# Kernel optimization log

Hardware: AMD Instinct MI355X
Metric: run time of the kernel (lower is better)

Reference implementation:

```python
import jax, jax.numpy as jnp
import numpy as np
import math

B, N, DIM = 16, 1024, 384
DEPTH, HEADS, DH = 6, 6, 64
INNER = HEADS * DH          # 384
MLP = 1536
LN_EPS = 1e-5


def setup_inputs() -> dict:
    key = jax.random.key(0)
    ks = jax.random.split(key, 7)
    s = 0.02
    x = jax.random.normal(ks[0], (B, N, DIM), dtype=jnp.float32)
    ln1_g = jnp.ones((DEPTH, DIM), jnp.float32)
    ln1_b = jnp.zeros((DEPTH, DIM), jnp.float32)
    qkv_w = jax.random.normal(ks[1], (DEPTH, DIM, 3 * INNER), jnp.float32) * s
    temp = jnp.full((DEPTH,), math.log(DH ** -0.5), jnp.float32)
    out_w = jax.random.normal(ks[2], (DEPTH, INNER, DIM), jnp.float32) * s
    out_b = jnp.zeros((DEPTH, DIM), jnp.float32)
    ln2_g = jnp.ones((DEPTH, DIM), jnp.float32)
    ln2_b = jnp.zeros((DEPTH, DIM), jnp.float32)
    ff_w1 = jax.random.normal(ks[3], (DEPTH, DIM, MLP), jnp.float32) * s
    ff_b1 = jnp.zeros((DEPTH, MLP), jnp.float32)
    ff_w2 = jax.random.normal(ks[4], (DEPTH, MLP, DIM), jnp.float32) * s
    ff_b2 = jnp.zeros((DEPTH, DIM), jnp.float32)
    return dict(x=x, ln1_g=ln1_g, ln1_b=ln1_b, qkv_w=qkv_w, temp=temp,
                out_w=out_w, out_b=out_b, ln2_g=ln2_g, ln2_b=ln2_b,
                ff_w1=ff_w1, ff_b1=ff_b1, ff_w2=ff_w2, ff_b2=ff_b2)


def _ln(x, g, b):
    m = jnp.mean(x, axis=-1, keepdims=True)
    v = jnp.var(x, axis=-1, keepdims=True)
    return (x - m) * jax.lax.rsqrt(v + LN_EPS) * g + b


def reference(x, ln1_g, ln1_b, qkv_w, temp, out_w, out_b,
              ln2_g, ln2_b, ff_w1, ff_b1, ff_w2, ff_b2):
    neg = -jnp.finfo(x.dtype).max
    eye = jnp.eye(N, dtype=bool)

    def step(x, p):
        g1, b1, wqkv, t, wo, bo, g2, b2, w1, bb1, w2, bb2 = p
        # --- PreNorm + LSA attention ---
        h = _ln(x, g1, b1)
        qkv = h @ wqkv                              # [B, N, 3*INNER]
        q, k, v = jnp.split(qkv, 3, axis=-1)
        split_heads = lambda a: a.reshape(B, N, HEADS, DH).transpose(0, 2, 1, 3)
        q, k, v = split_heads(q), split_heads(k), split_heads(v)
        dots = jnp.einsum('bhnd,bhmd->bhnm', q, k) * jnp.exp(t)
        dots = jnp.where(eye, neg, dots)            # mask diagonal (LSA)
        attn = jax.nn.softmax(dots, axis=-1)
        o = jnp.einsum('bhnm,bhmd->bhnd', attn, v)
        o = o.transpose(0, 2, 1, 3).reshape(B, N, INNER)
        x = x + o @ wo + bo
        # --- PreNorm + FeedForward (exact GELU) ---
        h2 = _ln(x, g2, b2)
        ff = jax.nn.gelu(h2 @ w1 + bb1, approximate=False) @ w2 + bb2
        x = x + ff
        return x, None

    params = (ln1_g, ln1_b, qkv_w, temp, out_w, out_b,
              ln2_g, ln2_b, ff_w1, ff_b1, ff_w2, ff_b2)
    x, _ = jax.lax.scan(step, x, params)
    return x
```

## Files before the change

### kernel.cpp

```cpp
#include <hip/hip_runtime.h>
#include <hip/hip_bf16.h>
#include <math.h>

#define B_     16
#define NTOK   1024
#define DIM_   384
#define DEPTH_ 6
#define HEADS_ 6
#define DH_    64
#define MLP_   1536
#define MTOT   (B_ * NTOK)
#define NBH    (B_ * HEADS_)
#define QKV_PLANE ((size_t)NBH * NTOK * DH_)

typedef unsigned short u16;
typedef unsigned int u32;
typedef short short8 __attribute__((ext_vector_type(8)));
typedef float f32x4 __attribute__((ext_vector_type(4)));

static __device__ __forceinline__ u16 f2b(float f) {
    __hip_bfloat16 h = __float2bfloat16(f);
    return *reinterpret_cast<u16*>(&h);
}

#define GLOAD_LDS16(gp, lp)                                                     \
    __builtin_amdgcn_global_load_lds(                                           \
        (const __attribute__((address_space(1))) void*)(gp),                    \
        (__attribute__((address_space(3))) void*)(lp), 16, 0, 0)

__launch_bounds__(256)
__global__ void transpose_w_kernel(const float* __restrict__ W, u16* __restrict__ WT,
                                   int K, int N) {
    const int layer = blockIdx.z;
    W  += (size_t)layer * K * N;
    WT += (size_t)layer * K * N;
    __shared__ u16 tile[64 * 72];
    const int t = threadIdx.x;
    const int k0 = blockIdx.x * 64, n0 = blockIdx.y * 64;
    const int row = t >> 2, cs = (t & 3) * 16;
    const float4* src = reinterpret_cast<const float4*>(W + (size_t)(k0 + row) * N + n0 + cs);
#pragma unroll
    for (int i = 0; i < 4; i++) {
        float4 f = src[i];
        tile[row * 72 + cs + i * 4 + 0] = f2b(f.x);
        tile[row * 72 + cs + i * 4 + 1] = f2b(f.y);
        tile[row * 72 + cs + i * 4 + 2] = f2b(f.z);
        tile[row * 72 + cs + i * 4 + 3] = f2b(f.w);
    }
    __syncthreads();
    const int nrow = row, ks = cs;
    u16 vals[16] __attribute__((aligned(16)));
#pragma unroll
    for (int e = 0; e < 16; e++) vals[e] = tile[(ks + e) * 72 + nrow];
    u16* dst = WT + (size_t)(n0 + nrow) * K + k0 + ks;
    *reinterpret_cast<short8*>(dst)     = *reinterpret_cast<short8*>(&vals[0]);
    *reinterpret_cast<short8*>(dst + 8) = *reinterpret_cast<short8*>(&vals[8]);
}

__launch_bounds__(256)
__global__ void ln_kernel(const float* __restrict__ x, const float* __restrict__ g,
                          const float* __restrict__ b, u16* __restrict__ h) {
    const int tok  = blockIdx.x * 4 + (threadIdx.x >> 6);
    const int lane = threadIdx.x & 63;
    const float* xr = x + (size_t)tok * DIM_;
    float v[6];
    float s = 0.f;
#pragma unroll
    for (int i = 0; i < 6; i++) { v[i] = xr[lane + i * 64]; s += v[i]; }
#pragma unroll
    for (int m = 1; m < 64; m <<= 1) s += __shfl_xor(s, m);
    const float mean = s * (1.f / 384.f);
    float qs = 0.f;
#pragma unroll
    for (int i = 0; i < 6; i++) { float d = v[i] - mean; qs += d * d; }
#pragma unroll
    for (int m = 1; m < 64; m <<= 1) qs += __shfl_xor(qs, m);
    const float inv = rsqrtf(qs * (1.f / 384.f) + 1e-5f);
    u16* hr = h + (size_t)tok * DIM_;
#pragma unroll
    for (int i = 0; i < 6; i++) {
        const int c = lane + i * 64;
        hr[c] = f2b((v[i] - mean) * inv * g[c] + b[c]);
    }
}

enum { EPI_QKV = 0, EPI_RES = 1, EPI_GELU = 2 };

template <int EPI>
__launch_bounds__(256)
__global__ void gemm_kernel(const u16* __restrict__ A, const u16* __restrict__ BT, int K,
                            const float* __restrict__ bias, const float* __restrict__ resid,
                            float* __restrict__ outf, u16* __restrict__ outb, int ldc,
                            u16* __restrict__ qkv_base) {
    __shared__ u16 As[128 * 32];
    __shared__ u16 Bs[128 * 32];
    const int t = threadIdx.x;
    const int lane = t & 63, w = t >> 6;
    const int wm = w >> 1, wn = w & 1;
    const int m0 = blockIdx.x * 128, n0 = blockIdx.y * 128;

    f32x4 acc[4][4] = {};

    const int c0 = w * 2, c1 = w * 2 + 1;
    const int seg = (lane & 3) * 8;
    const u16* agp0 = A  + (size_t)(m0 + c0 * 16 + (lane >> 2)) * K + seg;
    const u16* agp1 = A  + (size_t)(m0 + c1 * 16 + (lane >> 2)) * K + seg;
    const u16* bgp0 = BT + (size_t)(n0 + c0 * 16 + (lane >> 2)) * K + seg;
    const u16* bgp1 = BT + (size_t)(n0 + c1 * 16 + (lane >> 2)) * K + seg;
    u16* asl0 = &As[c0 * 512];
    u16* asl1 = &As[c1 * 512];
    u16* bsl0 = &Bs[c0 * 512];
    u16* bsl1 = &Bs[c1 * 512];

    for (int kk = 0; kk < K; kk += 32) {
        __syncthreads();
        GLOAD_LDS16(agp0 + kk, asl0);
        GLOAD_LDS16(agp1 + kk, asl1);
        GLOAD_LDS16(bgp0 + kk, bsl0);
        GLOAD_LDS16(bgp1 + kk, bsl1);
        __syncthreads();
        short8 af[4], bf[4];
#pragma unroll
        for (int i = 0; i < 4; i++)
            af[i] = *reinterpret_cast<const short8*>(
                &As[(wm * 64 + i * 16 + (lane & 15)) * 32 + (lane >> 4) * 8]);
#pragma unroll
        for (int j = 0; j < 4; j++)
            bf[j] = *reinterpret_cast<const short8*>(
                &Bs[(wn * 64 + j * 16 + (lane & 15)) * 32 + (lane >> 4) * 8]);
#pragma unroll
        for (int i = 0; i < 4; i++)
#pragma unroll
            for (int j = 0; j < 4; j++)
                acc[i][j] = __builtin_amdgcn_mfma_f32_16x16x32_bf16(af[i], bf[j], acc[i][j], 0, 0, 0);
    }

    const int rbase = (lane >> 4) * 4;
    const int cb = lane & 15;
#pragma unroll
    for (int i = 0; i < 4; i++) {
#pragma unroll
        for (int j = 0; j < 4; j++) {
            if constexpr (EPI == EPI_QKV) {
                const int c = n0 + wn * 64 + j * 16 + cb;
                const int which = c / 384;
                const int cc = c - which * 384;
                const int head = cc >> 6, dh = cc & 63;
                const int nb = m0 + wm * 64 + i * 16 + rbase;
                const int b = nb >> 10, nt = nb & 1023;
                const size_t bh = (size_t)(b * HEADS_ + head);
                if (which == 2) {
                    u16 pk[4] __attribute__((aligned(8)));
#pragma unroll
                    for (int r = 0; r < 4; r++) pk[r] = f2b(acc[i][j][r]);
                    const int nsw = (nt & ~63) | ((((nt >> 3) & 7) ^ (dh & 7)) << 3) | (nt & 7);
                    *reinterpret_cast<uint2*>(
                        &qkv_base[2 * QKV_PLANE + bh * 65536 + (size_t)dh * 1024 + nsw]) =
                        *reinterpret_cast<uint2*>(pk);
                } else if (which == 1) {
#pragma unroll
                    for (int r = 0; r < 4; r++) {
                        const int n = nt + r;
                        const int dsw = (((dh >> 3) ^ (n & 7)) << 3) | (dh & 7);
                        qkv_base[QKV_PLANE + bh * 65536 + (size_t)n * 64 + dsw] =
                            f2b(acc[i][j][r]);
                    }
                } else {
#pragma unroll
                    for (int r = 0; r < 4; r++)
                        qkv_base[bh * 65536 + (size_t)(nt + r) * 64 + dh] = f2b(acc[i][j][r]);
                }
            } else {
#pragma unroll
                for (int r = 0; r < 4; r++) {
                    const int m = m0 + wm * 64 + i * 16 + rbase + r;
                    const int c = n0 + wn * 64 + j * 16 + cb;
                    const float val = acc[i][j][r];
                    if constexpr (EPI == EPI_RES) {
                        outf[(size_t)m * ldc + c] = resid[(size_t)m * ldc + c] + bias[c] + val;
                    } else {
                        const float xg = val + bias[c];
                        const float ge = 0.5f * xg * (1.0f + erff(xg * 0.70710678118f));
                        outb[(size_t)m * ldc + c] = f2b(ge);
                    }
                }
            }
        }
    }
}

__launch_bounds__(256)
__global__ void attn_kernel(const u16* __restrict__ q, const u16* __restrict__ k,
                            const u16* __restrict__ v, const float* __restrict__ temp,
                            u16* __restrict__ o) {
    __shared__ u16 Kt[64 * 64];
    __shared__ u16 Vt[64 * 64];
    __shared__ u16 Ps[4][16 * 80];
    const int t = threadIdx.x, lane = t & 63, w = t >> 6;
    const int g8 = lane >> 4, qi = lane & 15;
    const int bh = blockIdx.x, q0 = blockIdx.y * 64;
    const float scale2 = __expf(temp[0]) * 1.4426950408889634f;
    const size_t base = (size_t)bh * (NTOK * DH_);

    short8 bq[2];
#pragma unroll
    for (int s = 0; s < 2; s++)
        bq[s] = *reinterpret_cast<const short8*>(
            &q[base + (size_t)(q0 + w * 16 + qi) * 64 + s * 32 + g8 * 8]);

    float m_s = -3.0e38f, l_s = 0.f;
    f32x4 accO[4] = {};
    const int qglob = q0 + w * 16 + qi;

    const int srow = w * 8 + (lane >> 3);
    const int schunk = (lane & 7) * 8;
    const u16* kg0 = k + base + (size_t)srow * 64 + schunk;
    const u16* vg0 = v + base + (size_t)srow * 1024 + schunk;
    u16* klds = &Kt[w * 512];
    u16* vlds = &Vt[w * 512];

    for (int j0 = 0; j0 < NTOK; j0 += 64) {
        __syncthreads();
        GLOAD_LDS16(kg0 + (size_t)j0 * 64,            klds);
        GLOAD_LDS16(kg0 + (size_t)j0 * 64 + 32 * 64,  klds + 2048);
        GLOAD_LDS16(vg0 + j0,                         vlds);
        GLOAD_LDS16(vg0 + j0 + 32 * 1024,             vlds + 2048);
        __syncthreads();

        f32x4 sf[4] = {};
#pragma unroll
        for (int c = 0; c < 4; c++) {
            const int krow = c * 16 + qi;
#pragma unroll
            for (int s = 0; s < 2; s++) {
                short8 af = *reinterpret_cast<const short8*>(
                    &Kt[krow * 64 + (((s * 4 + g8) ^ (krow & 7)) << 3)]);
                sf[c] = __builtin_amdgcn_mfma_f32_16x16x32_bf16(af, bq[s], sf[c], 0, 0, 0);
            }
        }

        float p[4][4];
        float vmax = -3.0e38f;
        if (j0 == q0) {
#pragma unroll
            for (int c = 0; c < 4; c++)
#pragma unroll
                for (int r = 0; r < 4; r++) {
                    float sv = sf[c][r] * scale2;
                    if (j0 + c * 16 + g8 * 4 + r == qglob) sv = -3.0e37f;
                    p[c][r] = sv;
                    vmax = fmaxf(vmax, sv);
                }
        } else {
#pragma unroll
            for (int c = 0; c < 4; c++)
#pragma unroll
                for (int r = 0; r < 4; r++) {
                    const float sv = sf[c][r] * scale2;
                    p[c][r] = sv;
                    vmax = fmaxf(vmax, sv);
                }
        }
        vmax = fmaxf(vmax, __shfl_xor(vmax, 16));
        vmax = fmaxf(vmax, __shfl_xor(vmax, 32));

        if (!__all(vmax - m_s <= 11.0f)) {
            const float mnew = fmaxf(m_s, vmax);
            const float alpha = exp2f(m_s - mnew);
            m_s = mnew;
            l_s *= alpha;
#pragma unroll
            for (int r = 0; r < 4; r++) {
                const float a_r = __shfl(alpha, g8 * 4 + r, 64);
#pragma unroll
                for (int g = 0; g < 4; g++) accO[g][r] *= a_r;
            }
        }

        float tsum = 0.f;
#pragma unroll
        for (int c = 0; c < 4; c++)
#pragma unroll
            for (int r = 0; r < 4; r++) {
                const float pe = exp2f(p[c][r] - m_s);
                p[c][r] = pe;
                tsum += pe;
            }
        tsum += __shfl_xor(tsum, 16);
        tsum += __shfl_xor(tsum, 32);
        l_s += tsum;

#pragma unroll
        for (int c = 0; c < 4; c++) {
            u32 lo = (u32)f2b(p[c][0]) | ((u32)f2b(p[c][1]) << 16);
            u32 hi = (u32)f2b(p[c][2]) | ((u32)f2b(p[c][3]) << 16);
            uint2 pr; pr.x = lo; pr.y = hi;
            *reinterpret_cast<uint2*>(&Ps[w][qi * 80 + c * 16 + g8 * 4]) = pr;
        }

#pragma unroll
        for (int s = 0; s < 2; s++) {
            short8 ap = *reinterpret_cast<const short8*>(&Ps[w][qi * 80 + s * 32 + g8 * 8]);
#pragma unroll
            for (int g = 0; g < 4; g++) {
                const int vrow = g * 16 + qi;
                short8 bv = *reinterpret_cast<const short8*>(
                    &Vt[vrow * 64 + (((s * 4 + g8) ^ (vrow & 7)) << 3)]);
                accO[g] = __builtin_amdgcn_mfma_f32_16x16x32_bf16(ap, bv, accO[g], 0, 0, 0);
            }
        }
    }

    const int bidx = bh / HEADS_, head = bh % HEADS_;
#pragma unroll
    for (int r = 0; r < 4; r++) {
        const float li = __shfl(l_s, g8 * 4 + r, 64);
        const float linv = 1.f / li;
        const int n = q0 + w * 16 + g8 * 4 + r;
#pragma unroll
        for (int g = 0; g < 4; g++) {
            const int dh = g * 16 + qi;
            o[((size_t)(bidx * NTOK + n)) * DIM_ + head * DH_ + dh] = f2b(accO[g][r] * linv);
        }
    }
}

extern "C" void kernel_launch(void* const* d_in, const int* in_sizes, int n_in,
                              void* d_out, int out_size, void* d_ws, size_t ws_size,
                              hipStream_t stream) {
    const float* x_in  = (const float*)d_in[0];
    const float* ln1_g = (const float*)d_in[1];
    const float* ln1_b = (const float*)d_in[2];
    const float* qkv_w = (const float*)d_in[3];
    const float* temp  = (const float*)d_in[4];
    const float* out_w = (const float*)d_in[5];
    const float* out_b = (const float*)d_in[6];
    const float* ln2_g = (const float*)d_in[7];
    const float* ln2_b = (const float*)d_in[8];
    const float* ff_w1 = (const float*)d_in[9];
    const float* ff_b1 = (const float*)d_in[10];
    const float* ff_w2 = (const float*)d_in[11];
    const float* ff_b2 = (const float*)d_in[12];

    char* ws = (char*)d_ws;
    size_t off = 0;
    auto alloc = [&](size_t bytes) -> void* {
        void* p = ws + off;
        off += (bytes + 255) & ~(size_t)255;
        return p;
    };
    u16* wt_qkv = (u16*)alloc((size_t)DEPTH_ * 1152 * 384 * 2);
    u16* wt_out = (u16*)alloc((size_t)DEPTH_ * 384 * 384 * 2);
    u16* wt_ff1 = (u16*)alloc((size_t)DEPTH_ * 1536 * 384 * 2);
    u16* wt_ff2 = (u16*)alloc((size_t)DEPTH_ * 384 * 1536 * 2);
    u16* H      = (u16*)alloc((size_t)MTOT * DIM_ * 2);
    u16* QKV    = (u16*)alloc((size_t)MTOT * MLP_ * 2);
    u16* MID    = QKV;

    float* X = (float*)d_out;

    hipMemcpyAsync(X, x_in, (size_t)MTOT * DIM_ * sizeof(float),
                   hipMemcpyDeviceToDevice, stream);

    transpose_w_kernel<<<dim3(6, 18, DEPTH_), 256, 0, stream>>>(qkv_w, wt_qkv, 384, 1152);
    transpose_w_kernel<<<dim3(6, 6, DEPTH_), 256, 0, stream>>>(out_w, wt_out, 384, 384);
    transpose_w_kernel<<<dim3(6, 24, DEPTH_), 256, 0, stream>>>(ff_w1, wt_ff1, 384, 1536);
    transpose_w_kernel<<<dim3(24, 6, DEPTH_), 256, 0, stream>>>(ff_w2, wt_ff2, 1536, 384);

    for (int layer = 0; layer < DEPTH_; layer++) {
        ln_kernel<<<4096, 256, 0, stream>>>(X, ln1_g + layer * DIM_, ln1_b + layer * DIM_, H);
        gemm_kernel<EPI_QKV><<<dim3(128, 9), 256, 0, stream>>>(
            H, wt_qkv + (size_t)layer * 1152 * 384, 384,
            nullptr, nullptr, nullptr, nullptr, 0, QKV);
        attn_kernel<<<dim3(96, 16), 256, 0, stream>>>(
            QKV, QKV + QKV_PLANE, QKV + 2 * QKV_PLANE, temp + layer, H);
        gemm_kernel<EPI_RES><<<dim3(128, 3), 256, 0, stream>>>(
            H, wt_out + (size_t)layer * 384 * 384, 384,
            out_b + layer * DIM_, X, X, nullptr, DIM_, nullptr);
        ln_kernel<<<4096, 256, 0, stream>>>(X, ln2_g + layer * DIM_, ln2_b + layer * DIM_, H);
        gemm_kernel<EPI_GELU><<<dim3(128, 12), 256, 0, stream>>>(
            H, wt_ff1 + (size_t)layer * 1536 * 384, 384,
            ff_b1 + layer * MLP_, nullptr, nullptr, MID, MLP_, nullptr);
        gemm_kernel<EPI_RES><<<dim3(128, 3), 256, 0, stream>>>(
            MID, wt_ff2 + (size_t)layer * 384 * 1536, 1536,
            ff_b2 + layer * DIM_, X, X, nullptr, DIM_, nullptr);
    }
}
```

Baseline: 1.388 ms.

## Multi-buffer LDS loads in GEMM and attention to overlap global loads with MFMA

After: 1.371 ms. Within noise of the previous version (-1.2%).

```diff
diff --git a/kernel.cpp b/kernel.cpp
--- a/kernel.cpp
+++ b/kernel.cpp
@@ -27,6 +27,13 @@
     __builtin_amdgcn_global_load_lds(                                           \
         (const __attribute__((address_space(1))) void*)(gp),                    \
         (__attribute__((address_space(3))) void*)(lp), 16, 0, 0)
+
+#define WAIT_VM(N)                                                              \
+    do { asm volatile("s_waitcnt vmcnt(" #N ")" ::: "memory");                  \
+         __builtin_amdgcn_sched_barrier(0); } while (0)
+#define WAIT_LGKM0()                                                            \
+    do { asm volatile("s_waitcnt lgkmcnt(0)" ::: "memory");                     \
+         __builtin_amdgcn_sched_barrier(0); } while (0)
 
 __launch_bounds__(256)
 __global__ void transpose_w_kernel(const float* __restrict__ W, u16* __restrict__ WT,
@@ -92,8 +99,8 @@
                             const float* __restrict__ bias, const float* __restrict__ resid,
                             float* __restrict__ outf, u16* __restrict__ outb, int ldc,
                             u16* __restrict__ qkv_base) {
-    __shared__ u16 As[128 * 32];
-    __shared__ u16 Bs[128 * 32];
+    __shared__ u16 As[3][4096];
+    __shared__ u16 Bs[3][4096];
     const int t = threadIdx.x;
     const int lane = t & 63, w = t >> 6;
     const int wm = w >> 1, wn = w & 1;
@@ -101,38 +108,55 @@
 
     f32x4 acc[4][4] = {};
 
-    const int c0 = w * 2, c1 = w * 2 + 1;
+    const int c0p = w * 1024, c1p = w * 1024 + 512;
     const int seg = (lane & 3) * 8;
-    const u16* agp0 = A  + (size_t)(m0 + c0 * 16 + (lane >> 2)) * K + seg;
-    const u16* agp1 = A  + (size_t)(m0 + c1 * 16 + (lane >> 2)) * K + seg;
-    const u16* bgp0 = BT + (size_t)(n0 + c0 * 16 + (lane >> 2)) * K + seg;
-    const u16* bgp1 = BT + (size_t)(n0 + c1 * 16 + (lane >> 2)) * K + seg;
-    u16* asl0 = &As[c0 * 512];
-    u16* asl1 = &As[c1 * 512];
-    u16* bsl0 = &Bs[c0 * 512];
-    u16* bsl1 = &Bs[c1 * 512];
-
-    for (int kk = 0; kk < K; kk += 32) {
-        __syncthreads();
-        GLOAD_LDS16(agp0 + kk, asl0);
-        GLOAD_LDS16(agp1 + kk, asl1);
-        GLOAD_LDS16(bgp0 + kk, bsl0);
-        GLOAD_LDS16(bgp1 + kk, bsl1);
-        __syncthreads();
+    const u16* agp0 = A  + (size_t)(m0 + (w * 2 + 0) * 16 + (lane >> 2)) * K + seg;
+    const u16* agp1 = A  + (size_t)(m0 + (w * 2 + 1) * 16 + (lane >> 2)) * K + seg;
+    const u16* bgp0 = BT + (size_t)(n0 + (w * 2 + 0) * 16 + (lane >> 2)) * K + seg;
+    const u16* bgp1 = BT + (size_t)(n0 + (w * 2 + 1) * 16 + (lane >> 2)) * K + seg;
+
+    const int T = K >> 5;
+    GLOAD_LDS16(agp0,      &As[0][c0p]);
+    GLOAD_LDS16(agp1,      &As[0][c1p]);
+    GLOAD_LDS16(bgp0,      &Bs[0][c0p]);
+    GLOAD_LDS16(bgp1,      &Bs[0][c1p]);
+    GLOAD_LDS16(agp0 + 32, &As[1][c0p]);
+    GLOAD_LDS16(agp1 + 32, &As[1][c1p]);
+    GLOAD_LDS16(bgp0 + 32, &Bs[1][c0p]);
+    GLOAD_LDS16(bgp1 + 32, &Bs[1][c1p]);
+
+    int b0 = 0, b1 = 1, b2 = 2;
+    for (int tt = 0; tt < T; ++tt) {
+        if (tt + 2 < T) {
+            const int kk = (tt + 2) << 5;
+            GLOAD_LDS16(agp0 + kk, &As[b2][c0p]);
+            GLOAD_LDS16(agp1 + kk, &As[b2][c1p]);
+            GLOAD_LDS16(bgp0 + kk, &Bs[b2][c0p]);
+            GLOAD_LDS16(bgp1 + kk, &Bs[b2][c1p]);
+            WAIT_VM(8);
+        } else if (tt + 1 < T) {
+            WAIT_VM(4);
+        } else {
+            WAIT_VM(0);
+        }
+        __builtin_amdgcn_s_barrier();
         short8 af[4], bf[4];
 #pragma unroll
         for (int i = 0; i < 4; i++)
             af[i] = *reinterpret_cast<const short8*>(
-                &As[(wm * 64 + i * 16 + (lane & 15)) * 32 + (lane >> 4) * 8]);
+                &As[b0][(wm * 64 + i * 16 + (lane & 15)) * 32 + (lane >> 4) * 8]);
 #pragma unroll
         for (int j = 0; j < 4; j++)
             bf[j] = *reinterpret_cast<const short8*>(
-                &Bs[(wn * 64 + j * 16 + (lane & 15)) * 32 + (lane >> 4) * 8]);
+                &Bs[b0][(wn * 64 + j * 16 + (lane & 15)) * 32 + (lane >> 4) * 8]);
 #pragma unroll
         for (int i = 0; i < 4; i++)
 #pragma unroll
             for (int j = 0; j < 4; j++)
                 acc[i][j] = __builtin_amdgcn_mfma_f32_16x16x32_bf16(af[i], bf[j], acc[i][j], 0, 0, 0);
+        WAIT_LGKM0();
+        __builtin_amdgcn_s_barrier();
+        const int tmp = b0; b0 = b1; b1 = b2; b2 = tmp;
     }
 
     const int rbase = (lane >> 4) * 4;
@@ -193,8 +217,8 @@
 __global__ void attn_kernel(const u16* __restrict__ q, const u16* __restrict__ k,
                             const u16* __restrict__ v, const float* __restrict__ temp,
                             u16* __restrict__ o) {
-    __shared__ u16 Kt[64 * 64];
-    __shared__ u16 Vt[64 * 64];
+    __shared__ u16 Kt[2][4096];
+    __shared__ u16 Vt[2][4096];
     __shared__ u16 Ps[4][16 * 80];
     const int t = threadIdx.x, lane = t & 63, w = t >> 6;
     const int g8 = lane >> 4, qi = lane & 15;
@@ -216,16 +240,26 @@
     const int schunk = (lane & 7) * 8;
     const u16* kg0 = k + base + (size_t)srow * 64 + schunk;
     const u16* vg0 = v + base + (size_t)srow * 1024 + schunk;
-    u16* klds = &Kt[w * 512];
-    u16* vlds = &Vt[w * 512];
-
-    for (int j0 = 0; j0 < NTOK; j0 += 64) {
-        __syncthreads();
-        GLOAD_LDS16(kg0 + (size_t)j0 * 64,            klds);
-        GLOAD_LDS16(kg0 + (size_t)j0 * 64 + 32 * 64,  klds + 2048);
-        GLOAD_LDS16(vg0 + j0,                         vlds);
-        GLOAD_LDS16(vg0 + j0 + 32 * 1024,             vlds + 2048);
-        __syncthreads();
+    const int wp = w * 512;
+
+    GLOAD_LDS16(kg0,             &Kt[0][wp]);
+    GLOAD_LDS16(kg0 + 32 * 64,   &Kt[0][wp + 2048]);
+    GLOAD_LDS16(vg0,             &Vt[0][wp]);
+    GLOAD_LDS16(vg0 + 32 * 1024, &Vt[0][wp + 2048]);
+
+    int cur = 0;
+    for (int jt = 0; jt < 16; ++jt) {
+        if (jt + 1 < 16) {
+            const size_t jn = (size_t)(jt + 1) * 64;
+            GLOAD_LDS16(kg0 + jn * 64,            &Kt[cur ^ 1][wp]);
+            GLOAD_LDS16(kg0 + jn * 64 + 32 * 64,  &Kt[cur ^ 1][wp + 2048]);
+            GLOAD_LDS16(vg0 + jn,                 &Vt[cur ^ 1][wp]);
+            GLOAD_LDS16(vg0 + jn + 32 * 1024,     &Vt[cur ^ 1][wp + 2048]);
+            WAIT_VM(4);
+        } else {
+            WAIT_VM(0);
+        }
+        __builtin_amdgcn_s_barrier();
 
         f32x4 sf[4] = {};
 #pragma unroll
@@ -234,20 +268,20 @@
 #pragma unroll
             for (int s = 0; s < 2; s++) {
                 short8 af = *reinterpret_cast<const short8*>(
-                    &Kt[krow * 64 + (((s * 4 + g8) ^ (krow & 7)) << 3)]);
+                    &Kt[cur][krow * 64 + (((s * 4 + g8) ^ (krow & 7)) << 3)]);
                 sf[c] = __builtin_amdgcn_mfma_f32_16x16x32_bf16(af, bq[s], sf[c], 0, 0, 0);
             }
         }
 
         float p[4][4];
         float vmax = -3.0e38f;
-        if (j0 == q0) {
+        if (jt * 64 == q0) {
 #pragma unroll
             for (int c = 0; c < 4; c++)
 #pragma unroll
                 for (int r = 0; r < 4; r++) {
                     float sv = sf[c][r] * scale2;
-                    if (j0 + c * 16 + g8 * 4 + r == qglob) sv = -3.0e37f;
+                    if (jt * 64 + c * 16 + g8 * 4 + r == qglob) sv = -3.0e37f;
                     p[c][r] = sv;
                     vmax = fmaxf(vmax, sv);
                 }
@@ -305,10 +339,13 @@
             for (int g = 0; g < 4; g++) {
                 const int vrow = g * 16 + qi;
                 short8 bv = *reinterpret_cast<const short8*>(
-                    &Vt[vrow * 64 + (((s * 4 + g8) ^ (vrow & 7)) << 3)]);
+                    &Vt[cur][vrow * 64 + (((s * 4 + g8) ^ (vrow & 7)) << 3)]);
                 accO[g] = __builtin_amdgcn_mfma_f32_16x16x32_bf16(ap, bv, accO[g], 0, 0, 0);
             }
         }
+        WAIT_LGKM0();
+        __builtin_amdgcn_s_barrier();
+        cur ^= 1;
     }
 
     const int bidx = bh / HEADS_, head = bh % HEADS_;
```
